# Optimization experiments

Hardware: AMD Instinct MI355X
Metric: run time of the kernel (lower is better)

The kernel has to match this reference:

```python
import jax, jax.numpy as jnp
import numpy as np
import math

D_MODEL = 1024
N_HEADS = 16
BATCH = 2
SEQ = 2048

def setup_inputs() -> dict:
    key = jax.random.key(0)
    ks = jax.random.split(key, 5)
    d = D_MODEL
    lim_qkv = 1.0 / math.sqrt(d)
    x = jax.random.normal(ks[0], (BATCH, SEQ, d), dtype=jnp.float32)
    qkv_w = jax.random.uniform(ks[1], (3 * d, d), dtype=jnp.float32, minval=-lim_qkv, maxval=lim_qkv)
    qkv_b = jax.random.uniform(ks[2], (3 * d,), dtype=jnp.float32, minval=-lim_qkv, maxval=lim_qkv)
    out_w = jax.random.uniform(ks[3], (d, d), dtype=jnp.float32, minval=-lim_qkv, maxval=lim_qkv)
    out_b = jax.random.uniform(ks[4], (d,), dtype=jnp.float32, minval=-lim_qkv, maxval=lim_qkv)
    return {"x": x, "qkv_w": qkv_w, "qkv_b": qkv_b, "out_w": out_w, "out_b": out_b}

def reference(x, qkv_w, qkv_b, out_w, out_b):
    b, s, d = x.shape
    h = N_HEADS
    hd = d // h
    # note: original uses float division for scale: sqrt(in_features / n_heads)
    scale = math.sqrt(d / h)
    qkv = x @ qkv_w.T + qkv_b                      # [b, s, 3d]
    q, k, v = jnp.split(qkv, 3, axis=-1)           # each [b, s, d]
    def heads(t):
        return t.reshape(b, s, h, hd).transpose(0, 2, 1, 3)  # [b, h, s, hd]
    qh, kh, vh = heads(q), heads(k), heads(v)
    # faithful quirk: scores = k @ q^T (k as query, q as key)
    scores = jnp.einsum('bhid,bhjd->bhij', kh, qh) / scale   # [b, h, s, s]
    alpha = jax.nn.softmax(scores, axis=-1)
    attn = jnp.einsum('bhij,bhjd->bhid', alpha, vh)          # [b, h, s, hd]
    attn = attn.transpose(0, 2, 1, 3).reshape(b, s, d)       # [b, s, d]
    return attn @ out_w.T + out_b
```

## Files before the change

### kernel.cpp

```cpp
#include <hip/hip_runtime.h>
#include <hip/hip_fp16.h>

#define D_MODEL 1024
#define N_HEADS 16
#define HEAD_DIM 64
#define BATCH 2
#define SEQ 2048
#define ROWS (BATCH*SEQ)

#define K_SCALE 0.18033688011112042f

using h8v = __attribute__((ext_vector_type(8))) _Float16;
using h4v = __attribute__((ext_vector_type(4))) _Float16;
using g2v = __attribute__((ext_vector_type(2))) __fp16;
using g4v = __attribute__((ext_vector_type(4))) __fp16;
using f4v = __attribute__((ext_vector_type(4))) float;

__device__ __forceinline__ ushort f2h_u(float x) { return __half_as_ushort(__float2half(x)); }
__device__ __forceinline__ void splith(float x, ushort& h, ushort& l) {
    __half hh_ = __float2half(x);
    h = __half_as_ushort(hh_);
    l = f2h_u(x - __half2float(hh_));
}

__device__ __forceinline__ size_t fidx(int row, int k) {
    return ((size_t)((row >> 7) * 32 + (k >> 5)) << 12)
         + (size_t)(((row & 127) >> 4) << 9)
         + (size_t)(((row & 15) * 4 + ((k & 31) >> 3)) << 3) + (k & 7);
}

__device__ __forceinline__ void async_lds16(const ushort* g, ushort* l) {
    __builtin_amdgcn_global_load_lds(
        (const __attribute__((address_space(1))) unsigned int*)g,
        (__attribute__((address_space(3))) unsigned int*)l, 16, 0, 0);
}

__global__ __launch_bounds__(256)
void prep_kernel(const float* __restrict__ x, const float* __restrict__ qw,
                 const float* __restrict__ ow,
                 ushort* __restrict__ xh, ushort* __restrict__ qwh,
                 ushort* __restrict__ owh, ushort* __restrict__ owl)
{
    const int b = blockIdx.x, t = threadIdx.x;
    if (b < 4096) {
        const int i = b * 256 + t;
        const int row = i >> 8, k4 = (i & 255) * 4;
        const float4 v = ((const float4*)x)[i];
        ushort4 h;
        h.x = f2h_u(v.x); h.y = f2h_u(v.y); h.z = f2h_u(v.z); h.w = f2h_u(v.w);
        *(ushort4*)&xh[fidx(row, k4)] = h;
    } else if (b < 7168) {
        const int i = (b - 4096) * 256 + t;
        const int row = i >> 8, k4 = (i & 255) * 4;
        const float4 v = ((const float4*)qw)[i];
        ushort4 h;
        h.x = f2h_u(v.x); h.y = f2h_u(v.y); h.z = f2h_u(v.z); h.w = f2h_u(v.w);
        *(ushort4*)&qwh[fidx(row, k4)] = h;
    } else {
        const int i = (b - 7168) * 256 + t;
        const int row = i >> 8, k4 = (i & 255) * 4;
        const float4 v = ((const float4*)ow)[i];
        const size_t o = fidx(row, k4);
        ushort4 h, l;
        splith(v.x, h.x, l.x); splith(v.y, h.y, l.y);
        splith(v.z, h.z, l.z); splith(v.w, h.w, l.w);
        *(ushort4*)&owh[o] = h; *(ushort4*)&owl[o] = l;
    }
}

__global__ __launch_bounds__(256, 5)
void gemm_qkv(const ushort* __restrict__ Af, const ushort* __restrict__ Wf,
              const float* __restrict__ bias,
              ushort* __restrict__ Qh, ushort* __restrict__ Kh,
              ushort* __restrict__ Vt)
{
    __shared__ ushort sA[2][4096], sW[2][2048];
    const int t = threadIdx.x, lane = t & 63, wv = t >> 6;
    const int tx = lane & 15, g = lane >> 4;
    const int lin = blockIdx.x;
    const int xcd = lin & 7, r = lin >> 3;
    const int mb = xcd * 4 + (r & 3);
    const int nb = r >> 2;
    const int at0 = (wv >> 1) * 4, wt0 = (wv & 1) * 2;
    const int fo = (tx * 4 + g) * 8;
    const size_t wbase = ((size_t)(nb & 1)) << 11;

    f4v acc[8];
#pragma unroll
    for (int i = 0; i < 8; i++)
#pragma unroll
        for (int e = 0; e < 4; e++) acc[i][e] = 0.f;

    {
        const size_t ao = ((size_t)(mb * 32)) << 12;
        const size_t wo = (((size_t)((nb >> 1) * 32)) << 12) + wbase;
#pragma unroll
        for (int c = 0; c < 2; c++) {
            const int o = (t + c * 256) * 8;
            async_lds16(Af + ao + o, &sA[0][o]);
        }
        async_lds16(Wf + wo + t * 8, &sW[0][t * 8]);
    }

    for (int kt = 0; kt < 32; kt++) {
        const int p = kt & 1;
        __syncthreads();
        if (kt < 31) {
            const size_t ao = ((size_t)(mb * 32 + kt + 1)) << 12;
            const size_t wo = (((size_t)((nb >> 1) * 32 + kt + 1)) << 12) + wbase;
#pragma unroll
            for (int c = 0; c < 2; c++) {
                const int o = (t + c * 256) * 8;
                async_lds16(Af + ao + o, &sA[p ^ 1][o]);
            }
            async_lds16(Wf + wo + t * 8, &sW[p ^ 1][t * 8]);
        }
        h8v ah[4], wh[2];
#pragma unroll
        for (int i = 0; i < 4; i++)
            ah[i] = *(const h8v*)&sA[p][(at0 + i) * 512 + fo];
#pragma unroll
        for (int i = 0; i < 2; i++)
            wh[i] = *(const h8v*)&sW[p][(wt0 + i) * 512 + fo];
        if (nb < 32) {
#pragma unroll
            for (int wi = 0; wi < 2; wi++)
#pragma unroll
                for (int ai = 0; ai < 4; ai++)
                    acc[wi * 4 + ai] = __builtin_amdgcn_mfma_f32_16x16x32_f16(wh[wi], ah[ai], acc[wi * 4 + ai], 0, 0, 0);
        } else {
#pragma unroll
            for (int ai = 0; ai < 4; ai++)
#pragma unroll
                for (int wi = 0; wi < 2; wi++)
                    acc[ai * 2 + wi] = __builtin_amdgcn_mfma_f32_16x16x32_f16(ah[ai], wh[wi], acc[ai * 2 + wi], 0, 0, 0);
        }
    }

    if (nb < 32) {
        const int part = nb >> 4;
        ushort* dst = part ? Kh : Qh;
        const float scale = part ? K_SCALE : 1.0f;
#pragma unroll
        for (int wi = 0; wi < 2; wi++) {
            const int gf0 = nb * 64 + (wv & 1) * 32 + wi * 16 + g * 4;
            const float4 bv = *(const float4*)&bias[gf0];
            const int gfl = gf0 & 1023;
            const int hh = gfl >> 6;
            const int dd = gfl & 63;
#pragma unroll
            for (int ai = 0; ai < 4; ai++) {
                const int s = mb * 128 + (wv >> 1) * 64 + ai * 16 + tx;
                const int bb = s >> 11, srel = s & 2047;
                const size_t idx = (size_t)(bb * N_HEADS + hh) * 131072
                    + (size_t)(srel >> 4) * 1024 + (size_t)(dd >> 5) * 512
                    + ((srel & 15) * 4 + ((dd & 31) >> 3)) * 8 + (dd & 7);
                const f4v a = acc[wi * 4 + ai];
                ushort4 h4;
                h4.x = f2h_u((a[0] + bv.x) * scale);
                h4.y = f2h_u((a[1] + bv.y) * scale);
                h4.z = f2h_u((a[2] + bv.z) * scale);
                h4.w = f2h_u((a[3] + bv.w) * scale);
                *(ushort4*)&dst[idx] = h4;
            }
        }
    } else {
#pragma unroll
        for (int wi = 0; wi < 2; wi++) {
            const int gf = nb * 64 + (wv & 1) * 32 + wi * 16 + tx;
            const float bv = bias[gf];
            const int gfl = gf & 1023;
            const int hh = gfl >> 6;
            const int dl = gfl & 63;
#pragma unroll
            for (int ai = 0; ai < 4; ai++) {
                const int jt0 = mb * 128 + (wv >> 1) * 64 + ai * 16 + g * 4;
                const int bb = jt0 >> 11, jr = jt0 & 2047;
                const int jj = jr & 63;
                const size_t idx = (size_t)(bb * N_HEADS + hh) * 131072
                    + (size_t)(jr >> 6) * 4096
                    + (size_t)(jj >> 5) * 2048
                    + (size_t)((dl >> 4) & 3) * 512
                    + (size_t)((jj >> 2) & 3) * 128
                    + (size_t)(dl & 15) * 8
                    + (size_t)((jj >> 4) & 1) * 4;
                const f4v a = acc[ai * 2 + wi];
                ushort4 h4;
                h4.x = f2h_u(a[0] + bv);
                h4.y = f2h_u(a[1] + bv);
                h4.z = f2h_u(a[2] + bv);
                h4.w = f2h_u(a[3] + bv);
                *(ushort4*)&Vt[idx] = h4;
            }
        }
    }
}

__global__ __launch_bounds__(256)
void attn_mfma(const ushort* __restrict__ Kf, const ushort* __restrict__ Qf,
               const ushort* __restrict__ Vf,
               ushort* __restrict__ Oh, ushort* __restrict__ Ol)
{
    __shared__ ushort lds[32768];
    ushort* KR = lds;
    ushort* bufs = lds + 8192;

    const int t = threadIdx.x, lane = t & 63, wv = t >> 6;
    const int tx = lane & 15, g = lane >> 4;
    const int lin = blockIdx.x;
    const int xcd = lin & 7, ix = lin >> 3;
    const int bh = xcd * 4 + (ix >> 4);
    const int it = ix & 15;
    const int b = bh >> 4, h = bh & 15;
    const int i0 = it * 128;
    const size_t hb = (size_t)bh * 131072;

    {
        const size_t kb = hb + (size_t)it * 8192;
#pragma unroll
        for (int c = 0; c < 4; c++) {
            const int o = (t + c * 256) * 8;
            async_lds16(Kf + kb + o, KR + o);
        }
#pragma unroll
        for (int c = 0; c < 2; c++) {
            const int o = (t + c * 256) * 8;
            async_lds16(Qf + hb + o, bufs + o);
            async_lds16(Vf + hb + o, bufs + 4096 + o);
        }
    }
    __syncthreads();

    const int fo = (tx * 4 + g) * 8;
    const int vo = (g * 16 + tx) * 8;
    h8v kf[2][2];
#pragma unroll
    for (int is = 0; is < 2; is++)
#pragma unroll
        for (int kk = 0; kk < 2; kk++)
            kf[is][kk] = *(const h8v*)&KR[((wv * 2 + is) * 2 + kk) * 512 + fo];

    {
        const size_t off = hb + 4096;
#pragma unroll
        for (int c = 0; c < 2; c++) {
            const int o = (t + c * 256) * 8;
            async_lds16(Qf + off + o, bufs + 8192 + o);
            async_lds16(Vf + off + o, bufs + 8192 + 4096 + o);
        }
    }

    f4v O[2][4];
    float l_acc[2] = {0.f, 0.f};
#pragma unroll
    for (int is = 0; is < 2; is++)
#pragma unroll
        for (int ht = 0; ht < 4; ht++)
#pragma unroll
            for (int e = 0; e < 4; e++) O[is][ht][e] = 0.f;

    h4v php[2][4];

    {
        const ushort* sQ = bufs;
        f4v sc[2][4];
#pragma unroll
        for (int is = 0; is < 2; is++)
#pragma unroll
            for (int jn = 0; jn < 4; jn++)
#pragma unroll
                for (int e = 0; e < 4; e++) sc[is][jn][e] = 0.f;
#pragma unroll
        for (int kk = 0; kk < 2; kk++)
#pragma unroll
            for (int jn = 0; jn < 4; jn++) {
                const h8v qf = *(const h8v*)&sQ[(jn * 2 + kk) * 512 + fo];
#pragma unroll
                for (int is = 0; is < 2; is++)
                    sc[is][jn] = __builtin_amdgcn_mfma_f32_16x16x32_f16(qf, kf[is][kk], sc[is][jn], 0, 0, 0);
            }
#pragma unroll
        for (int is = 0; is < 2; is++)
#pragma unroll
            for (int jn = 0; jn < 4; jn++) {
                const float p0 = __builtin_amdgcn_exp2f(sc[is][jn][0]);
                const float p1 = __builtin_amdgcn_exp2f(sc[is][jn][1]);
                const float p2 = __builtin_amdgcn_exp2f(sc[is][jn][2]);
                const float p3 = __builtin_amdgcn_exp2f(sc[is][jn][3]);
                l_acc[is] += (p0 + p1) + (p2 + p3);
                const g2v plo = __builtin_amdgcn_cvt_pkrtz(p0, p1);
                const g2v phi = __builtin_amdgcn_cvt_pkrtz(p2, p3);
                const g4v pk = __builtin_shufflevector(plo, phi, 0, 1, 2, 3);
                php[is][jn] = __builtin_bit_cast(h4v, pk);
            }
    }

    int bp = 0, bc = 1, bn = 2;
    for (int jt = 1; jt < SEQ / 64; jt++) {
        __syncthreads();
        if (jt < SEQ / 64 - 1) {
            const size_t off = hb + (size_t)(jt + 1) * 4096;
#pragma unroll
            for (int c = 0; c < 2; c++) {
                const int o = (t + c * 256) * 8;
                async_lds16(Qf + off + o, bufs + bn * 8192 + o);
                async_lds16(Vf + off + o, bufs + bn * 8192 + 4096 + o);
            }
        }
        const ushort* sQ = bufs + bc * 8192;
        const ushort* sVp = bufs + bp * 8192 + 4096;

        f4v sc[2][4];
#pragma unroll
        for (int is = 0; is < 2; is++)
#pragma unroll
            for (int jn = 0; jn < 4; jn++)
#pragma unroll
                for (int e = 0; e < 4; e++) sc[is][jn][e] = 0.f;
#pragma unroll
        for (int kk = 0; kk < 2; kk++)
#pragma unroll
            for (int jn = 0; jn < 4; jn++) {
                const h8v qf = *(const h8v*)&sQ[(jn * 2 + kk) * 512 + fo];
#pragma unroll
                for (int is = 0; is < 2; is++)
                    sc[is][jn] = __builtin_amdgcn_mfma_f32_16x16x32_f16(qf, kf[is][kk], sc[is][jn], 0, 0, 0);
            }

#pragma unroll
        for (int jc = 0; jc < 2; jc++) {
            h8v p8[2];
#pragma unroll
            for (int is = 0; is < 2; is++)
                p8[is] = __builtin_shufflevector(php[is][jc * 2], php[is][jc * 2 + 1],
                                                 0, 1, 2, 3, 4, 5, 6, 7);
#pragma unroll
            for (int ht = 0; ht < 4; ht++) {
                const h8v vf = *(const h8v*)&sVp[jc * 2048 + ht * 512 + vo];
#pragma unroll
                for (int is = 0; is < 2; is++)
                    O[is][ht] = __builtin_amdgcn_mfma_f32_16x16x32_f16(vf, p8[is], O[is][ht], 0, 0, 0);
            }
        }

#pragma unroll
        for (int is = 0; is < 2; is++)
#pragma unroll
            for (int jn = 0; jn < 4; jn++) {
                const float p0 = __builtin_amdgcn_exp2f(sc[is][jn][0]);
                const float p1 = __builtin_amdgcn_exp2f(sc[is][jn][1]);
                const float p2 = __builtin_amdgcn_exp2f(sc[is][jn][2]);
                const float p3 = __builtin_amdgcn_exp2f(sc[is][jn][3]);
                l_acc[is] += (p0 + p1) + (p2 + p3);
                const g2v plo = __builtin_amdgcn_cvt_pkrtz(p0, p1);
                const g2v phi = __builtin_amdgcn_cvt_pkrtz(p2, p3);
                const g4v pk = __builtin_shufflevector(plo, phi, 0, 1, 2, 3);
                php[is][jn] = __builtin_bit_cast(h4v, pk);
            }

        const int tmp = bp; bp = bc; bc = bn; bn = tmp;
    }

    {
        const ushort* sVp = bufs + bp * 8192 + 4096;
#pragma unroll
        for (int jc = 0; jc < 2; jc++) {
            h8v p8[2];
#pragma unroll
            for (int is = 0; is < 2; is++)
                p8[is] = __builtin_shufflevector(php[is][jc * 2], php[is][jc * 2 + 1],
                                                 0, 1, 2, 3, 4, 5, 6, 7);
#pragma unroll
            for (int ht = 0; ht < 4; ht++) {
                const h8v vf = *(const h8v*)&sVp[jc * 2048 + ht * 512 + vo];
#pragma unroll
                for (int is = 0; is < 2; is++)
                    O[is][ht] = __builtin_amdgcn_mfma_f32_16x16x32_f16(vf, p8[is], O[is][ht], 0, 0, 0);
            }
        }
    }

#pragma unroll
    for (int is = 0; is < 2; is++) {
        float l = l_acc[is];
        l += __shfl_xor(l, 16);
        l += __shfl_xor(l, 32);
        const float inv = 1.0f / l;
        const int row = b * SEQ + i0 + (wv * 2 + is) * 16 + tx;
#pragma unroll
        for (int ht = 0; ht < 4; ht++) {
            const int k0 = h * 64 + ht * 16 + g * 4;
            const size_t o = fidx(row, k0);
            ushort4 hv, lv;
            float v;
            v = O[is][ht][0] * inv; splith(v, hv.x, lv.x);
            v = O[is][ht][1] * inv; splith(v, hv.y, lv.y);
            v = O[is][ht][2] * inv; splith(v, hv.z, lv.z);
            v = O[is][ht][3] * inv; splith(v, hv.w, lv.w);
            *(ushort4*)&Oh[o] = hv;
            *(ushort4*)&Ol[o] = lv;
        }
    }
}

__global__ __launch_bounds__(256, 4)
void gemm_out(const ushort* __restrict__ Af, const ushort* __restrict__ Alf,
              const ushort* __restrict__ Wf, const ushort* __restrict__ Wlf,
              const float* __restrict__ bias, float* __restrict__ out)
{
    __shared__ ushort sA[2][4096], sW[2][4096];
    const int t = threadIdx.x, lane = t & 63, wv = t >> 6;
    const int tx = lane & 15, g = lane >> 4;
    const int lin = blockIdx.x;
    const int xcd = lin & 7, r = lin >> 3;
    const int nb = xcd * 2 + (r & 1);
    const int mb = r >> 1;
    const int at0 = (wv >> 1) * 2, wt0 = (wv & 1) * 2;
    const int fo = (tx * 4 + g) * 8;
    const size_t abase = ((size_t)(mb & 1)) << 11;
    const size_t wbase = ((size_t)(nb & 1)) << 11;

    f4v acc[4];
#pragma unroll
    for (int i = 0; i < 4; i++)
#pragma unroll
        for (int e = 0; e < 4; e++) acc[i][e] = 0.f;

    {
        const size_t ao = (((size_t)((mb >> 1) * 32)) << 12) + abase;
        const size_t wo = (((size_t)((nb >> 1) * 32)) << 12) + wbase;
        const int o = t * 8;
        async_lds16(Af + ao + o, &sA[0][o]);
        async_lds16(Alf + ao + o, &sA[0][2048 + o]);
        async_lds16(Wf + wo + o, &sW[0][o]);
        async_lds16(Wlf + wo + o, &sW[0][2048 + o]);
    }

    for (int kt = 0; kt < 32; kt++) {
        const int p = kt & 1;
        __syncthreads();
        if (kt < 31) {
            const size_t ao = (((size_t)((mb >> 1) * 32 + kt + 1)) << 12) + abase;
            const size_t wo = (((size_t)((nb >> 1) * 32 + kt + 1)) << 12) + wbase;
            const int o = t * 8;
            async_lds16(Af + ao + o, &sA[p ^ 1][o]);
            async_lds16(Alf + ao + o, &sA[p ^ 1][2048 + o]);
            async_lds16(Wf + wo + o, &sW[p ^ 1][o]);
            async_lds16(Wlf + wo + o, &sW[p ^ 1][2048 + o]);
        }
        h8v ah[2], al[2], wh[2], wl[2];
#pragma unroll
        for (int i = 0; i < 2; i++) {
            ah[i] = *(const h8v*)&sA[p][(at0 + i) * 512 + fo];
            al[i] = *(const h8v*)&sA[p][2048 + (at0 + i) * 512 + fo];
            wh[i] = *(const h8v*)&sW[p][(wt0 + i) * 512 + fo];
            wl[i] = *(const h8v*)&sW[p][2048 + (wt0 + i) * 512 + fo];
        }
#pragma unroll
        for (int wi = 0; wi < 2; wi++)
#pragma unroll
            for (int ai = 0; ai < 2; ai++) {
                acc[wi * 2 + ai] = __builtin_amdgcn_mfma_f32_16x16x32_f16(wh[wi], ah[ai], acc[wi * 2 + ai], 0, 0, 0);
                acc[wi * 2 + ai] = __builtin_amdgcn_mfma_f32_16x16x32_f16(wh[wi], al[ai], acc[wi * 2 + ai], 0, 0, 0);
                acc[wi * 2 + ai] = __builtin_amdgcn_mfma_f32_16x16x32_f16(wl[wi], ah[ai], acc[wi * 2 + ai], 0, 0, 0);
            }
    }

#pragma unroll
    for (int wi = 0; wi < 2; wi++) {
        const int gf0 = nb * 64 + (wv & 1) * 32 + wi * 16 + g * 4;
        const float4 bv = *(const float4*)&bias[gf0];
#pragma unroll
        for (int ai = 0; ai < 2; ai++) {
            const int tok = mb * 64 + (wv >> 1) * 32 + ai * 16 + tx;
            const f4v a = acc[wi * 2 + ai];
            float4 o;
            o.x = a[0] + bv.x;
            o.y = a[1] + bv.y;
            o.z = a[2] + bv.z;
            o.w = a[3] + bv.w;
            *(float4*)&out[(size_t)tok * D_MODEL + gf0] = o;
        }
    }
}

extern "C" void kernel_launch(void* const* d_in, const int* in_sizes, int n_in,
                              void* d_out, int out_size, void* d_ws, size_t ws_size,
                              hipStream_t stream) {
    const float* x     = (const float*)d_in[0];
    const float* qkv_w = (const float*)d_in[1];
    const float* qkv_b = (const float*)d_in[2];
    const float* out_w = (const float*)d_in[3];
    const float* out_b = (const float*)d_in[4];
    float* out = (float*)d_out;

    const size_t FB = (size_t)ROWS * D_MODEL;
    const size_t MM = (size_t)D_MODEL * D_MODEL;
    ushort* u   = (ushort*)d_ws;
    ushort* xh  = u;
    ushort* Ol  = u + FB;
    ushort* Qh  = u + 2 * FB;
    ushort* Kh  = u + 3 * FB;
    ushort* Vt  = u + 4 * FB;
    ushort* qwh = u + 5 * FB;
    ushort* owh = u + 5 * FB + 3 * MM;
    ushort* owl = owh + MM;

    prep_kernel<<<8192, 256, 0, stream>>>(x, qkv_w, out_w, xh, qwh, owh, owl);
    gemm_qkv<<<1536, 256, 0, stream>>>(xh, qwh, qkv_b, Qh, Kh, Vt);
    attn_mfma<<<512, 256, 0, stream>>>(Kh, Qh, Vt, xh, Ol);
    gemm_out<<<1024, 256, 0, stream>>>(xh, Ol, owh, owl, out_b, out);
}
```

Measured before the change: 207.2 us.

## Triple-buffer LDS tiles in QKV and output GEMMs with two-stage prefetch

Both projection GEMMs move from double to triple LDS buffering and prefetch two K-tiles ahead. The __syncthreads is replaced by an explicit s_waitcnt vmcnt(N) plus s_barrier, so only the oldest tile's loads must land before compute starts. This is meant to hide global-load latency behind MFMA work, at the cost of more LDS per block and a lower occupancy hint in launch_bounds (5 to 4 and 4 to 3).

```diff
diff --git a/kernel.cpp b/kernel.cpp
--- a/kernel.cpp
+++ b/kernel.cpp
@@ -68,13 +68,13 @@
     }
 }
 
-__global__ __launch_bounds__(256, 5)
+__global__ __launch_bounds__(256, 4)
 void gemm_qkv(const ushort* __restrict__ Af, const ushort* __restrict__ Wf,
               const float* __restrict__ bias,
               ushort* __restrict__ Qh, ushort* __restrict__ Kh,
               ushort* __restrict__ Vt)
 {
-    __shared__ ushort sA[2][4096], sW[2][2048];
+    __shared__ ushort sA[3][4096], sW[3][2048];
     const int t = threadIdx.x, lane = t & 63, wv = t >> 6;
     const int tx = lane & 15, g = lane >> 4;
     const int lin = blockIdx.x;
@@ -91,37 +91,41 @@
 #pragma unroll
         for (int e = 0; e < 4; e++) acc[i][e] = 0.f;
 
-    {
-        const size_t ao = ((size_t)(mb * 32)) << 12;
-        const size_t wo = (((size_t)((nb >> 1) * 32)) << 12) + wbase;
+#pragma unroll
+    for (int k0 = 0; k0 < 2; k0++) {
+        const size_t ao = ((size_t)(mb * 32 + k0)) << 12;
+        const size_t wo = (((size_t)((nb >> 1) * 32 + k0)) << 12) + wbase;
 #pragma unroll
         for (int c = 0; c < 2; c++) {
             const int o = (t + c * 256) * 8;
-            async_lds16(Af + ao + o, &sA[0][o]);
-        }
-        async_lds16(Wf + wo + t * 8, &sW[0][t * 8]);
-    }
-
+            async_lds16(Af + ao + o, &sA[k0][o]);
+        }
+        async_lds16(Wf + wo + t * 8, &sW[k0][t * 8]);
+    }
+
+    int cur = 0;
     for (int kt = 0; kt < 32; kt++) {
-        const int p = kt & 1;
-        __syncthreads();
-        if (kt < 31) {
-            const size_t ao = ((size_t)(mb * 32 + kt + 1)) << 12;
-            const size_t wo = (((size_t)((nb >> 1) * 32 + kt + 1)) << 12) + wbase;
+        if (kt == 31) asm volatile("s_waitcnt vmcnt(0)" ::: "memory");
+        else          asm volatile("s_waitcnt vmcnt(3)" ::: "memory");
+        asm volatile("s_barrier" ::: "memory");
+        if (kt < 30) {
+            const int nxt = (cur >= 1) ? cur - 1 : 2;
+            const size_t ao = ((size_t)(mb * 32 + kt + 2)) << 12;
+            const size_t wo = (((size_t)((nb >> 1) * 32 + kt + 2)) << 12) + wbase;
 #pragma unroll
             for (int c = 0; c < 2; c++) {
                 const int o = (t + c * 256) * 8;
-                async_lds16(Af + ao + o, &sA[p ^ 1][o]);
-            }
-            async_lds16(Wf + wo + t * 8, &sW[p ^ 1][t * 8]);
+                async_lds16(Af + ao + o, &sA[nxt][o]);
+            }
+            async_lds16(Wf + wo + t * 8, &sW[nxt][t * 8]);
         }
         h8v ah[4], wh[2];
 #pragma unroll
         for (int i = 0; i < 4; i++)
-            ah[i] = *(const h8v*)&sA[p][(at0 + i) * 512 + fo];
+            ah[i] = *(const h8v*)&sA[cur][(at0 + i) * 512 + fo];
 #pragma unroll
         for (int i = 0; i < 2; i++)
-            wh[i] = *(const h8v*)&sW[p][(wt0 + i) * 512 + fo];
+            wh[i] = *(const h8v*)&sW[cur][(wt0 + i) * 512 + fo];
         if (nb < 32) {
 #pragma unroll
             for (int wi = 0; wi < 2; wi++)
@@ -135,6 +139,7 @@
                 for (int wi = 0; wi < 2; wi++)
                     acc[ai * 2 + wi] = __builtin_amdgcn_mfma_f32_16x16x32_f16(ah[ai], wh[wi], acc[ai * 2 + wi], 0, 0, 0);
         }
+        cur = (cur == 2) ? 0 : cur + 1;
     }
 
     if (nb < 32) {
@@ -403,12 +408,12 @@
     }
 }
 
-__global__ __launch_bounds__(256, 4)
+__global__ __launch_bounds__(256, 3)
 void gemm_out(const ushort* __restrict__ Af, const ushort* __restrict__ Alf,
               const ushort* __restrict__ Wf, const ushort* __restrict__ Wlf,
               const float* __restrict__ bias, float* __restrict__ out)
 {
-    __shared__ ushort sA[2][4096], sW[2][4096];
+    __shared__ ushort sA[3][4096], sW[3][4096];
     const int t = threadIdx.x, lane = t & 63, wv = t >> 6;
     const int tx = lane & 15, g = lane >> 4;
     const int lin = blockIdx.x;
@@ -426,35 +431,39 @@
 #pragma unroll
         for (int e = 0; e < 4; e++) acc[i][e] = 0.f;
 
-    {
-        const size_t ao = (((size_t)((mb >> 1) * 32)) << 12) + abase;
-        const size_t wo = (((size_t)((nb >> 1) * 32)) << 12) + wbase;
+#pragma unroll
+    for (int k0 = 0; k0 < 2; k0++) {
+        const size_t ao = (((size_t)((mb >> 1) * 32 + k0)) << 12) + abase;
+        const size_t wo = (((size_t)((nb >> 1) * 32 + k0)) << 12) + wbase;
         const int o = t * 8;
-        async_lds16(Af + ao + o, &sA[0][o]);
-        async_lds16(Alf + ao + o, &sA[0][2048 + o]);
-        async_lds16(Wf + wo + o, &sW[0][o]);
-        async_lds16(Wlf + wo + o, &sW[0][2048 + o]);
-    }
-
+        async_lds16(Af + ao + o, &sA[k0][o]);
+        async_lds16(Alf + ao + o, &sA[k0][2048 + o]);
+        async_lds16(Wf + wo + o, &sW[k0][o]);
+        async_lds16(Wlf + wo + o, &sW[k0][2048 + o]);
+    }
+
+    int cur = 0;
     for (int kt = 0; kt < 32; kt++) {
-        const int p = kt & 1;
-        __syncthreads();
-        if (kt < 31) {
-            const size_t ao = (((size_t)((mb >> 1) * 32 + kt + 1)) << 12) + abase;
-            const size_t wo = (((size_t)((nb >> 1) * 32 + kt + 1)) << 12) + wbase;
+        if (kt == 31) asm volatile("s_waitcnt vmcnt(0)" ::: "memory");
+        else          asm volatile("s_waitcnt vmcnt(4)" ::: "memory");
+        asm volatile("s_barrier" ::: "memory");
+        if (kt < 30) {
+            const int nxt = (cur >= 1) ? cur - 1 : 2;
+            const size_t ao = (((size_t)((mb >> 1) * 32 + kt + 2)) << 12) + abase;
+            const size_t wo = (((size_t)((nb >> 1) * 32 + kt + 2)) << 12) + wbase;
             const int o = t * 8;
-            async_lds16(Af + ao + o, &sA[p ^ 1][o]);
-            async_lds16(Alf + ao + o, &sA[p ^ 1][2048 + o]);
-            async_lds16(Wf + wo + o, &sW[p ^ 1][o]);
-            async_lds16(Wlf + wo + o, &sW[p ^ 1][2048 + o]);
+            async_lds16(Af + ao + o, &sA[nxt][o]);
+            async_lds16(Alf + ao + o, &sA[nxt][2048 + o]);
+            async_lds16(Wf + wo + o, &sW[nxt][o]);
+            async_lds16(Wlf + wo + o, &sW[nxt][2048 + o]);
         }
         h8v ah[2], al[2], wh[2], wl[2];
 #pragma unroll
         for (int i = 0; i < 2; i++) {
-            ah[i] = *(const h8v*)&sA[p][(at0 + i) * 512 + fo];
-            al[i] = *(const h8v*)&sA[p][2048 + (at0 + i) * 512 + fo];
-            wh[i] = *(const h8v*)&sW[p][(wt0 + i) * 512 + fo];
-            wl[i] = *(const h8v*)&sW[p][2048 + (wt0 + i) * 512 + fo];
+            ah[i] = *(const h8v*)&sA[cur][(at0 + i) * 512 + fo];
+            al[i] = *(const h8v*)&sA[cur][2048 + (at0 + i) * 512 + fo];
+            wh[i] = *(const h8v*)&sW[cur][(wt0 + i) * 512 + fo];
+            wl[i] = *(const h8v*)&sW[cur][2048 + (wt0 + i) * 512 + fo];
         }
 #pragma unroll
         for (int wi = 0; wi < 2; wi++)
@@ -464,6 +473,7 @@
                 acc[wi * 2 + ai] = __builtin_amdgcn_mfma_f32_16x16x32_f16(wh[wi], al[ai], acc[wi * 2 + ai], 0, 0, 0);
                 acc[wi * 2 + ai] = __builtin_amdgcn_mfma_f32_16x16x32_f16(wl[wi], ah[ai], acc[wi * 2 + ai], 0, 0, 0);
             }
+        cur = (cur == 2) ? 0 : cur + 1;
     }
 
 #pragma unroll
```

After: 219.5 us. 1.06x slower.
